# Performance work log

Hardware: AMD Instinct MI355X
Metric: run time of the kernel (lower is better)

## Reference

```python
import jax, jax.numpy as jnp
import numpy as np

BETA = 0.25
NUM_EMBEDS = 1024
EMBED_DIM = 256


def setup_inputs() -> dict:
    key = jax.random.key(0)
    k1, k2 = jax.random.split(key)
    z_e = jax.random.normal(k1, (32, EMBED_DIM, 1024), dtype=jnp.float32)
    lim = 1.0 / NUM_EMBEDS
    embed_weight = jax.random.uniform(k2, (NUM_EMBEDS, EMBED_DIM), dtype=jnp.float32,
                                      minval=-lim, maxval=lim)
    return {"z_e": z_e, "embed_weight": embed_weight}


def reference(z_e, embed_weight):
    # z_e: (b, d, t) -> (b, t, d)
    ze = jnp.transpose(z_e, (0, 2, 1))
    b, t, d = ze.shape
    flat = ze.reshape(-1, d)  # (N, d)
    K = embed_weight.shape[0]
    # squared euclidean distances (N, K) via sum-of-squares + matmul
    distances = (jnp.sum(flat ** 2, axis=1, keepdims=True)
                 + jnp.sum(embed_weight ** 2, axis=1)
                 - 2.0 * flat @ embed_weight.T)
    idx = jnp.argmin(distances, axis=1)  # (N,)
    # one-hot @ W is just a gather
    z_q = embed_weight[idx].reshape(b, t, d)
    # commitment / codebook losses (mse over all elements)
    e_latent_loss = jnp.mean((jax.lax.stop_gradient(z_q) - ze) ** 2)
    q_latent_loss = jnp.mean((z_q - jax.lax.stop_gradient(ze)) ** 2)
    reg_loss = q_latent_loss + BETA * e_latent_loss
    # straight-through estimator
    z_q_st = ze + jax.lax.stop_gradient(z_q - ze)
    z_q_out = jnp.transpose(z_q_st, (0, 2, 1))  # (b, d, t)
    # perplexity from codebook usage
    N = flat.shape[0]
    avg_probs = jnp.zeros((K,), dtype=jnp.float32).at[idx].add(1.0) / N
    perplexity = jnp.exp(-jnp.sum(avg_probs * jnp.log(avg_probs + 1e-10)))
    return (z_q_out, reg_loss, perplexity)
```

## Files before the change

### kernel.cpp

```cpp
#include <hip/hip_runtime.h>
#include <math.h>

#define BB 32
#define DD 256
#define TT 1024
#define KK 1024
#define NN (BB*TT)

#define BROWS 128
#define NSTEP 32


__global__ void prep_kernel(const float* __restrict__ W, float* __restrict__ wsq,
                            int* __restrict__ counts, float* __restrict__ sse) {
    const int k = blockIdx.x;
    const int lane = threadIdx.x;
    const float4 v = ((const float4*)(W + (size_t)k * DD))[lane];
    double s = (double)v.x * v.x + (double)v.y * v.y + (double)v.z * v.z + (double)v.w * v.w;
    #pragma unroll
    for (int m = 32; m > 0; m >>= 1) s += __shfl_down(s, m);
    if (lane == 0) wsq[k] = (float)s;
    if (blockIdx.x < 16) counts[blockIdx.x * 64 + lane] = 0;
    if (blockIdx.x == 0 && lane == 0) *sse = 0.0f;
}

__device__ __forceinline__ void gl_lds16(const float* g, void* l) {
    __builtin_amdgcn_global_load_lds((const __attribute__((address_space(1))) void*)g,
                                     (__attribute__((address_space(3))) void*)l, 16, 0, 0);
}

__global__ __launch_bounds__(512, 2) void vq_fused_kernel(
    const float* __restrict__ z, const float* __restrict__ W,
    const float* __restrict__ wsq, float* __restrict__ out,
    int* __restrict__ counts, float* __restrict__ sse)
{
    __shared__ float zst[2][16 * 128];
    __shared__ float wst[2][16 * 512];
    __shared__ float rsql[128];
    const int tid = threadIdx.x;
    const int wid = tid >> 6, lane = tid & 63;
    const int row0 = blockIdx.x * BROWS;
    const int b = row0 >> 10, t0 = row0 & 1023;
    const size_t bbase = (size_t)b * DD * TT;
    const float* zbase = z + bbase + t0;

    {
        char* dw = (char*)&wst[0][0];
        #pragma unroll
        for (int k = 0; k < 4; ++k) {
            const int m = k * 512 + tid;
            const int j = m >> 8, q = (m >> 6) & 3, l = m & 63;
            gl_lds16(W + (size_t)(j * 64 + l) * DD + q * 4, dw + (size_t)m * 16);
        }
        const int d = tid >> 5, r4 = (tid & 31) * 4;
        gl_lds16(zbase + (size_t)d * TT + r4, (char*)&zst[0][0] + (size_t)tid * 16);
    }

    {
        double* pscr = (double*)&zst[1][0];
        const int rr = tid & 127, g = tid >> 7;
        const float* zp = zbase + (size_t)g * 64 * TT + rr;
        double s = 0.0;
        #pragma unroll 4
        for (int d = 0; d < 64; ++d) { float v = zp[(size_t)d * TT]; s += (double)v * v; }
        pscr[g * 128 + rr] = s;
        __syncthreads();
        if (tid < 128)
            rsql[tid] = (float)((pscr[tid] + pscr[128 + tid]) + (pscr[256 + tid] + pscr[384 + tid]));
    }

    float minv[16]; int mini[16];
    #pragma unroll
    for (int i = 0; i < 16; ++i) { minv[i] = 3.4e38f; mini[i] = 0; }
    float acc[16][8];

    for (int t = 0; t < NSTEP; ++t) {
        const int ch = t >> 4, sl = t & 15, h = t & 1;
        __syncthreads();
        if (t + 1 < NSTEP) {
            const int tn = t + 1, chn = tn >> 4, sln = tn & 15;
            const float* wc = W + (size_t)(chn * 512) * DD + sln * 16;
            char* dw = (char*)&wst[tn & 1][0];
            #pragma unroll
            for (int k = 0; k < 4; ++k) {
                const int m = k * 512 + tid;
                const int j = m >> 8, q = (m >> 6) & 3, l = m & 63;
                gl_lds16(wc + (size_t)(j * 64 + l) * DD + q * 4, dw + (size_t)m * 16);
            }
            const int d = tid >> 5, r4 = (tid & 31) * 4;
            gl_lds16(zbase + (size_t)(sln * 16 + d) * TT + r4,
                     (char*)&zst[tn & 1][0] + (size_t)tid * 16);
        }
        if (sl == 0) {
            #pragma unroll
            for (int i = 0; i < 16; ++i)
                #pragma unroll
                for (int j = 0; j < 8; ++j) acc[i][j] = 0.0f;
        }
        const float*  zb  = &zst[h][0];
        const float4* wb4 = (const float4*)&wst[h][0];
        __builtin_amdgcn_s_setprio(1);
        #pragma clang loop unroll(disable)
        for (int q = 0; q < 4; ++q) {
            const float4* wp = wb4 + q * 64 + lane;
            float4 wf[8];
            #pragma unroll
            for (int j = 0; j < 8; ++j) wf[j] = wp[j * 256];
            #pragma unroll
            for (int dp = 0; dp < 4; ++dp) {
                const float4* zp4 = (const float4*)(zb + (q * 4 + dp) * 128 + wid * 16);
                const float4 za = zp4[0], zc = zp4[1], ze = zp4[2], zg = zp4[3];
                #pragma unroll
                for (int j = 0; j < 8; ++j) {
                    const float wv = dp == 0 ? wf[j].x : dp == 1 ? wf[j].y
                                   : dp == 2 ? wf[j].z : wf[j].w;
                    acc[0][j]  = fmaf(za.x, wv, acc[0][j]);
                    acc[1][j]  = fmaf(za.y, wv, acc[1][j]);
                    acc[2][j]  = fmaf(za.z, wv, acc[2][j]);
                    acc[3][j]  = fmaf(za.w, wv, acc[3][j]);
                    acc[4][j]  = fmaf(zc.x, wv, acc[4][j]);
                    acc[5][j]  = fmaf(zc.y, wv, acc[5][j]);
                    acc[6][j]  = fmaf(zc.z, wv, acc[6][j]);
                    acc[7][j]  = fmaf(zc.w, wv, acc[7][j]);
                    acc[8][j]  = fmaf(ze.x, wv, acc[8][j]);
                    acc[9][j]  = fmaf(ze.y, wv, acc[9][j]);
                    acc[10][j] = fmaf(ze.z, wv, acc[10][j]);
                    acc[11][j] = fmaf(ze.w, wv, acc[11][j]);
                    acc[12][j] = fmaf(zg.x, wv, acc[12][j]);
                    acc[13][j] = fmaf(zg.y, wv, acc[13][j]);
                    acc[14][j] = fmaf(zg.z, wv, acc[14][j]);
                    acc[15][j] = fmaf(zg.w, wv, acc[15][j]);
                }
            }
        }
        __builtin_amdgcn_s_setprio(0);
        if (sl == 15) {
            float wq[8];
            #pragma unroll
            for (int j = 0; j < 8; ++j) wq[j] = wsq[ch * 512 + j * 64 + lane];
            #pragma unroll
            for (int i = 0; i < 16; ++i) {
                const float rs = rsql[wid * 16 + i];
                #pragma unroll
                for (int j = 0; j < 8; ++j) {
                    const float s1 = rs + wq[j];
                    const float v = fmaf(-2.0f, acc[i][j], s1);
                    if (v < minv[i]) { minv[i] = v; mini[i] = ch * 512 + j * 64 + lane; }
                }
            }
        }
    }

    __syncthreads();
    int* idxs = (int*)&zst[0][0];
    float* ssescr = (float*)&wst[0][0];
    #pragma unroll
    for (int i = 0; i < 16; ++i) {
        float v = minv[i]; int ix = mini[i];
        #pragma unroll
        for (int m = 1; m < 64; m <<= 1) {
            float ov = __shfl_xor(v, m);
            int   oi = __shfl_xor(ix, m);
            if (ov < v || (ov == v && oi < ix)) { v = ov; ix = oi; }
        }
        if (lane == 0) {
            idxs[wid * 16 + i] = ix;
            atomicAdd(&counts[ix], 1);
        }
    }
    __syncthreads();

    const int tg = tid & 31;
    const int dg = tid >> 5;
    const int t4 = tg * 4;
    int ixs[4];
    #pragma unroll
    for (int m = 0; m < 4; ++m) ixs[m] = idxs[t4 + m];
    float ssel = 0.0f;
    #pragma unroll
    for (int k4 = 0; k4 < 4; ++k4) {
        const int d0 = dg * 16 + k4 * 4;
        float wr[4][4];
        #pragma unroll
        for (int m = 0; m < 4; ++m) {
            float4 wv = *(const float4*)(W + (size_t)ixs[m] * DD + d0);
            wr[m][0] = wv.x; wr[m][1] = wv.y; wr[m][2] = wv.z; wr[m][3] = wv.w;
        }
        #pragma unroll
        for (int dd = 0; dd < 4; ++dd) {
            const int d = d0 + dd;
            const size_t base = bbase + (size_t)d * TT + t0 + t4;
            float4 zv = *(const float4*)(z + base);
            float e0 = wr[0][dd] - zv.x, e1 = wr[1][dd] - zv.y;
            float e2 = wr[2][dd] - zv.z, e3 = wr[3][dd] - zv.w;
            float4 o;
            o.x = zv.x + e0; o.y = zv.y + e1; o.z = zv.z + e2; o.w = zv.w + e3;
            *(float4*)(out + base) = o;
            ssel += (e0 * e0 + e1 * e1) + (e2 * e2 + e3 * e3);
        }
    }
    #pragma unroll
    for (int m = 32; m > 0; m >>= 1) ssel += __shfl_down(ssel, m);
    if (lane == 0) ssescr[wid] = ssel;
    __syncthreads();
    if (tid == 0)
        atomicAdd(sse, ((ssescr[0] + ssescr[1]) + (ssescr[2] + ssescr[3]))
                     + ((ssescr[4] + ssescr[5]) + (ssescr[6] + ssescr[7])));
}

__global__ void finalize_kernel(const int* __restrict__ counts, const float* __restrict__ sse,
                                float* __restrict__ out) {
    float s = 0.0f;
    for (int k = threadIdx.x; k < KK; k += 256) {
        float p = (float)counts[k] / (float)NN;
        s += p * logf(p + 1e-10f);
    }
    #pragma unroll
    for (int m = 32; m > 0; m >>= 1) s += __shfl_down(s, m);
    __shared__ float wsum[4];
    if ((threadIdx.x & 63) == 0) wsum[threadIdx.x >> 6] = s;
    __syncthreads();
    if (threadIdx.x == 0) {
        float ent = (wsum[0] + wsum[1]) + (wsum[2] + wsum[3]);
        out[(size_t)BB * DD * TT]     = 1.25f * (*sse) / (float)(BB * DD * TT);
        out[(size_t)BB * DD * TT + 1] = expf(-ent);
    }
}

extern "C" void kernel_launch(void* const* d_in, const int* in_sizes, int n_in,
                              void* d_out, int out_size, void* d_ws, size_t ws_size,
                              hipStream_t stream) {
    const float* z = (const float*)d_in[0];
    const float* W = (const float*)d_in[1];
    float* out = (float*)d_out;

    float* wsq    = (float*)d_ws;
    int*   counts = (int*)(wsq + 1024);
    float* sse    = (float*)(counts + 1024);

    prep_kernel<<<1024, 64, 0, stream>>>(W, wsq, counts, sse);
    vq_fused_kernel<<<NN / BROWS, 512, 0, stream>>>(z, W, wsq, out, counts, sse);
    finalize_kernel<<<1, 256, 0, stream>>>(counts, sse, out);
}
```

Before: 228.5 us.

## Overlap row-norm computation with distance GEMM loop and unroll inner q loop

Removes the up-front strided loads that computed each row's squared norm before the main loop. The loads are now spread across the first 13 pipeline steps: issued before the FMA block and accumulated in double after it. Partial sums go to a dedicated LDS scratch and are reduced at step 13, before the first argmin at step 15. The inner q loop is also unrolled by two, which raises register pressure under the 512-thread, 2-block launch bounds and could cause spills.

```diff
diff --git a/kernel.cpp b/kernel.cpp
--- a/kernel.cpp
+++ b/kernel.cpp
@@ -36,6 +36,7 @@
 {
     __shared__ float zst[2][16 * 128];
     __shared__ float wst[2][16 * 512];
+    __shared__ double pscr[512];
     __shared__ float rsql[128];
     const int tid = threadIdx.x;
     const int wid = tid >> 6, lane = tid & 63;
@@ -56,18 +57,8 @@
         gl_lds16(zbase + (size_t)d * TT + r4, (char*)&zst[0][0] + (size_t)tid * 16);
     }
 
-    {
-        double* pscr = (double*)&zst[1][0];
-        const int rr = tid & 127, g = tid >> 7;
-        const float* zp = zbase + (size_t)g * 64 * TT + rr;
-        double s = 0.0;
-        #pragma unroll 4
-        for (int d = 0; d < 64; ++d) { float v = zp[(size_t)d * TT]; s += (double)v * v; }
-        pscr[g * 128 + rr] = s;
-        __syncthreads();
-        if (tid < 128)
-            rsql[tid] = (float)((pscr[tid] + pscr[128 + tid]) + (pscr[256 + tid] + pscr[384 + tid]));
-    }
+    const float* zrow = zbase + (size_t)(tid >> 7) * 64 * TT + (tid & 127);
+    double rchain = 0.0;
 
     float minv[16]; int mini[16];
     #pragma unroll
@@ -91,6 +82,19 @@
             gl_lds16(zbase + (size_t)(sln * 16 + d) * TT + r4,
                      (char*)&zst[tn & 1][0] + (size_t)tid * 16);
         }
+        float rv[5];
+        if (t < 13) {
+            #pragma unroll
+            for (int k = 0; k < 5; ++k) {
+                const int d = t * 5 + k;
+                if (d < 64) rv[k] = zrow[(size_t)d * TT];
+            }
+        }
+        if (sl == 13) {
+            if (tid < 128)
+                rsql[tid] = (float)((pscr[tid] + pscr[128 + tid])
+                                  + (pscr[256 + tid] + pscr[384 + tid]));
+        }
         if (sl == 0) {
             #pragma unroll
             for (int i = 0; i < 16; ++i)
@@ -100,7 +104,7 @@
         const float*  zb  = &zst[h][0];
         const float4* wb4 = (const float4*)&wst[h][0];
         __builtin_amdgcn_s_setprio(1);
-        #pragma clang loop unroll(disable)
+        #pragma clang loop unroll_count(2)
         for (int q = 0; q < 4; ++q) {
             const float4* wp = wb4 + q * 64 + lane;
             float4 wf[8];
@@ -134,6 +138,14 @@
             }
         }
         __builtin_amdgcn_s_setprio(0);
+        if (t < 13) {
+            #pragma unroll
+            for (int k = 0; k < 5; ++k) {
+                const int d = t * 5 + k;
+                if (d < 64) rchain += (double)rv[k] * rv[k];
+            }
+            if (t == 12) pscr[tid] = rchain;
+        }
         if (sl == 15) {
             float wq[8];
             #pragma unroll
```

Result: slower. 272.5 us (+19.3%).

## Triple-buffer LDS staging with explicit vmcnt waits and single barrier per step

Applied to the files above, without the earlier changes.

Moves the shared-memory staging of codebook and input slices from double to triple buffering, prefetching two steps ahead. Explicit s_waitcnt vmcnt counts plus a raw s_barrier at the end of each step replace the leading __syncthreads, so loads issued for later steps can stay in flight across the barrier. The codebook squared norms are loaded into registers once before the loop rather than at each chunk end. The extra buffer raises LDS use, which may limit residency of two blocks per CU, and the hand-counted vmcnt values must match the number of async loads issued.

```diff
diff --git a/kernel.cpp b/kernel.cpp
--- a/kernel.cpp
+++ b/kernel.cpp
@@ -34,8 +34,8 @@
     const float* __restrict__ wsq, float* __restrict__ out,
     int* __restrict__ counts, float* __restrict__ sse)
 {
-    __shared__ float zst[2][16 * 128];
-    __shared__ float wst[2][16 * 512];
+    __shared__ float zst[3][16 * 128];
+    __shared__ float wst[3][16 * 512];
     __shared__ float rsql[128];
     const int tid = threadIdx.x;
     const int wid = tid >> 6, lane = tid & 63;
@@ -44,20 +44,23 @@
     const size_t bbase = (size_t)b * DD * TT;
     const float* zbase = z + bbase + t0;
 
-    {
-        char* dw = (char*)&wst[0][0];
+    #pragma unroll
+    for (int pt = 0; pt < 2; ++pt) {
+        const float* wc = W + (size_t)0 * DD + pt * 16;
+        char* dw = (char*)&wst[pt][0];
         #pragma unroll
         for (int k = 0; k < 4; ++k) {
             const int m = k * 512 + tid;
             const int j = m >> 8, q = (m >> 6) & 3, l = m & 63;
-            gl_lds16(W + (size_t)(j * 64 + l) * DD + q * 4, dw + (size_t)m * 16);
+            gl_lds16(wc + (size_t)(j * 64 + l) * DD + q * 4, dw + (size_t)m * 16);
         }
         const int d = tid >> 5, r4 = (tid & 31) * 4;
-        gl_lds16(zbase + (size_t)d * TT + r4, (char*)&zst[0][0] + (size_t)tid * 16);
+        gl_lds16(zbase + (size_t)(pt * 16 + d) * TT + r4,
+                 (char*)&zst[pt][0] + (size_t)tid * 16);
     }
 
     {
-        double* pscr = (double*)&zst[1][0];
+        double* pscr = (double*)&wst[2][0];
         const int rr = tid & 127, g = tid >> 7;
         const float* zp = zbase + (size_t)g * 64 * TT + rr;
         double s = 0.0;
@@ -69,18 +72,27 @@
             rsql[tid] = (float)((pscr[tid] + pscr[128 + tid]) + (pscr[256 + tid] + pscr[384 + tid]));
     }
 
+    float wq0[8], wq1[8];
+    #pragma unroll
+    for (int j = 0; j < 8; ++j) {
+        wq0[j] = wsq[j * 64 + lane];
+        wq1[j] = wsq[512 + j * 64 + lane];
+    }
+
+    asm volatile("s_waitcnt vmcnt(0)" ::: "memory");
+    __syncthreads();
+
     float minv[16]; int mini[16];
     #pragma unroll
     for (int i = 0; i < 16; ++i) { minv[i] = 3.4e38f; mini[i] = 0; }
     float acc[16][8];
 
     for (int t = 0; t < NSTEP; ++t) {
-        const int ch = t >> 4, sl = t & 15, h = t & 1;
-        __syncthreads();
-        if (t + 1 < NSTEP) {
-            const int tn = t + 1, chn = tn >> 4, sln = tn & 15;
+        const int sl = t & 15, h = t % 3;
+        if (t + 2 < NSTEP) {
+            const int tn = t + 2, chn = tn >> 4, sln = tn & 15, hn = tn % 3;
             const float* wc = W + (size_t)(chn * 512) * DD + sln * 16;
-            char* dw = (char*)&wst[tn & 1][0];
+            char* dw = (char*)&wst[hn][0];
             #pragma unroll
             for (int k = 0; k < 4; ++k) {
                 const int m = k * 512 + tid;
@@ -89,7 +101,7 @@
             }
             const int d = tid >> 5, r4 = (tid & 31) * 4;
             gl_lds16(zbase + (size_t)(sln * 16 + d) * TT + r4,
-                     (char*)&zst[tn & 1][0] + (size_t)tid * 16);
+                     (char*)&zst[hn][0] + (size_t)tid * 16);
         }
         if (sl == 0) {
             #pragma unroll
@@ -134,21 +146,32 @@
             }
         }
         __builtin_amdgcn_s_setprio(0);
-        if (sl == 15) {
-            float wq[8];
-            #pragma unroll
-            for (int j = 0; j < 8; ++j) wq[j] = wsq[ch * 512 + j * 64 + lane];
+        if (t == 15) {
             #pragma unroll
             for (int i = 0; i < 16; ++i) {
                 const float rs = rsql[wid * 16 + i];
                 #pragma unroll
                 for (int j = 0; j < 8; ++j) {
-                    const float s1 = rs + wq[j];
+                    const float s1 = rs + wq0[j];
                     const float v = fmaf(-2.0f, acc[i][j], s1);
-                    if (v < minv[i]) { minv[i] = v; mini[i] = ch * 512 + j * 64 + lane; }
+                    if (v < minv[i]) { minv[i] = v; mini[i] = j * 64 + lane; }
                 }
             }
-        }
+        } else if (t == 31) {
+            #pragma unroll
+            for (int i = 0; i < 16; ++i) {
+                const float rs = rsql[wid * 16 + i];
+                #pragma unroll
+                for (int j = 0; j < 8; ++j) {
+                    const float s1 = rs + wq1[j];
+                    const float v = fmaf(-2.0f, acc[i][j], s1);
+                    if (v < minv[i]) { minv[i] = v; mini[i] = 512 + j * 64 + lane; }
+                }
+            }
+        }
+        if (t + 2 < NSTEP) { asm volatile("s_waitcnt vmcnt(5)" ::: "memory"); }
+        else               { asm volatile("s_waitcnt vmcnt(0)" ::: "memory"); }
+        __builtin_amdgcn_s_barrier();
     }
 
     __syncthreads();
```

Result: slower. 289.9 us (+26.9%).

## Double block to 1024 threads, halve per-thread rows, reduce argmin per chunk

Applied to the files above, without the earlier changes.

Launches the fused VQ kernel with 1024 threads per block. Each wave now owns 8 rows instead of 16, so the accumulator shrinks from 16x8 to 8x8 registers and occupancy can rise. The argmin across lanes now runs once per 512-code chunk, and the two chunk results are merged through shared memory, which removes the per-row running min registers. In exchange, each thread does less FMA work per LDS read of the W fragment, so the arithmetic intensity per LDS load drops, and the launch bounds of (1024,4) impose tight register limits that may cause spills.

```diff
diff --git a/kernel.cpp b/kernel.cpp
--- a/kernel.cpp
+++ b/kernel.cpp
@@ -29,7 +29,7 @@
                                      (__attribute__((address_space(3))) void*)l, 16, 0, 0);
 }
 
-__global__ __launch_bounds__(512, 2) void vq_fused_kernel(
+__global__ __launch_bounds__(1024, 4) void vq_fused_kernel(
     const float* __restrict__ z, const float* __restrict__ W,
     const float* __restrict__ wsq, float* __restrict__ out,
     int* __restrict__ counts, float* __restrict__ sse)
@@ -37,6 +37,9 @@
     __shared__ float zst[2][16 * 128];
     __shared__ float wst[2][16 * 512];
     __shared__ float rsql[128];
+    __shared__ float c0v[128];
+    __shared__ int   c0i[128];
+    __shared__ int   idxs[128];
     const int tid = threadIdx.x;
     const int wid = tid >> 6, lane = tid & 63;
     const int row0 = blockIdx.x * BROWS;
@@ -47,32 +50,33 @@
     {
         char* dw = (char*)&wst[0][0];
         #pragma unroll
-        for (int k = 0; k < 4; ++k) {
-            const int m = k * 512 + tid;
+        for (int k = 0; k < 2; ++k) {
+            const int m = k * 1024 + tid;
             const int j = m >> 8, q = (m >> 6) & 3, l = m & 63;
             gl_lds16(W + (size_t)(j * 64 + l) * DD + q * 4, dw + (size_t)m * 16);
         }
-        const int d = tid >> 5, r4 = (tid & 31) * 4;
-        gl_lds16(zbase + (size_t)d * TT + r4, (char*)&zst[0][0] + (size_t)tid * 16);
+        if (tid < 512) {
+            const int d = tid >> 5, r4 = (tid & 31) * 4;
+            gl_lds16(zbase + (size_t)d * TT + r4, (char*)&zst[0][0] + (size_t)tid * 16);
+        }
     }
 
     {
         double* pscr = (double*)&zst[1][0];
-        const int rr = tid & 127, g = tid >> 7;
-        const float* zp = zbase + (size_t)g * 64 * TT + rr;
-        double s = 0.0;
-        #pragma unroll 4
-        for (int d = 0; d < 64; ++d) { float v = zp[(size_t)d * TT]; s += (double)v * v; }
-        pscr[g * 128 + rr] = s;
+        if (tid < 512) {
+            const int rr = tid & 127, g = (tid >> 7) & 3;
+            const float* zp = zbase + (size_t)g * 64 * TT + rr;
+            double s = 0.0;
+            #pragma unroll 4
+            for (int d = 0; d < 64; ++d) { float v = zp[(size_t)d * TT]; s += (double)v * v; }
+            pscr[g * 128 + rr] = s;
+        }
         __syncthreads();
         if (tid < 128)
             rsql[tid] = (float)((pscr[tid] + pscr[128 + tid]) + (pscr[256 + tid] + pscr[384 + tid]));
     }
 
-    float minv[16]; int mini[16];
-    #pragma unroll
-    for (int i = 0; i < 16; ++i) { minv[i] = 3.4e38f; mini[i] = 0; }
-    float acc[16][8];
+    float acc[8][8];
 
     for (int t = 0; t < NSTEP; ++t) {
         const int ch = t >> 4, sl = t & 15, h = t & 1;
@@ -82,18 +86,20 @@
             const float* wc = W + (size_t)(chn * 512) * DD + sln * 16;
             char* dw = (char*)&wst[tn & 1][0];
             #pragma unroll
-            for (int k = 0; k < 4; ++k) {
-                const int m = k * 512 + tid;
+            for (int k = 0; k < 2; ++k) {
+                const int m = k * 1024 + tid;
                 const int j = m >> 8, q = (m >> 6) & 3, l = m & 63;
                 gl_lds16(wc + (size_t)(j * 64 + l) * DD + q * 4, dw + (size_t)m * 16);
             }
-            const int d = tid >> 5, r4 = (tid & 31) * 4;
-            gl_lds16(zbase + (size_t)(sln * 16 + d) * TT + r4,
-                     (char*)&zst[tn & 1][0] + (size_t)tid * 16);
+            if (tid < 512) {
+                const int d = tid >> 5, r4 = (tid & 31) * 4;
+                gl_lds16(zbase + (size_t)(sln * 16 + d) * TT + r4,
+                         (char*)&zst[tn & 1][0] + (size_t)tid * 16);
+            }
         }
         if (sl == 0) {
             #pragma unroll
-            for (int i = 0; i < 16; ++i)
+            for (int i = 0; i < 8; ++i)
                 #pragma unroll
                 for (int j = 0; j < 8; ++j) acc[i][j] = 0.0f;
         }
@@ -108,28 +114,20 @@
             for (int j = 0; j < 8; ++j) wf[j] = wp[j * 256];
             #pragma unroll
             for (int dp = 0; dp < 4; ++dp) {
-                const float4* zp4 = (const float4*)(zb + (q * 4 + dp) * 128 + wid * 16);
-                const float4 za = zp4[0], zc = zp4[1], ze = zp4[2], zg = zp4[3];
+                const float4* zp4 = (const float4*)(zb + (q * 4 + dp) * 128 + wid * 8);
+                const float4 za = zp4[0], zc = zp4[1];
                 #pragma unroll
                 for (int j = 0; j < 8; ++j) {
                     const float wv = dp == 0 ? wf[j].x : dp == 1 ? wf[j].y
                                    : dp == 2 ? wf[j].z : wf[j].w;
-                    acc[0][j]  = fmaf(za.x, wv, acc[0][j]);
-                    acc[1][j]  = fmaf(za.y, wv, acc[1][j]);
-                    acc[2][j]  = fmaf(za.z, wv, acc[2][j]);
-                    acc[3][j]  = fmaf(za.w, wv, acc[3][j]);
-                    acc[4][j]  = fmaf(zc.x, wv, acc[4][j]);
-                    acc[5][j]  = fmaf(zc.y, wv, acc[5][j]);
-                    acc[6][j]  = fmaf(zc.z, wv, acc[6][j]);
-                    acc[7][j]  = fmaf(zc.w, wv, acc[7][j]);
-                    acc[8][j]  = fmaf(ze.x, wv, acc[8][j]);
-                    acc[9][j]  = fmaf(ze.y, wv, acc[9][j]);
-                    acc[10][j] = fmaf(ze.z, wv, acc[10][j]);
-                    acc[11][j] = fmaf(ze.w, wv, acc[11][j]);
-                    acc[12][j] = fmaf(zg.x, wv, acc[12][j]);
-                    acc[13][j] = fmaf(zg.y, wv, acc[13][j]);
-                    acc[14][j] = fmaf(zg.z, wv, acc[14][j]);
-                    acc[15][j] = fmaf(zg.w, wv, acc[15][j]);
+                    acc[0][j] = fmaf(za.x, wv, acc[0][j]);
+                    acc[1][j] = fmaf(za.y, wv, acc[1][j]);
+                    acc[2][j] = fmaf(za.z, wv, acc[2][j]);
+                    acc[3][j] = fmaf(za.w, wv, acc[3][j]);
+                    acc[4][j] = fmaf(zc.x, wv, acc[4][j]);
+                    acc[5][j] = fmaf(zc.y, wv, acc[5][j]);
+                    acc[6][j] = fmaf(zc.z, wv, acc[6][j]);
+                    acc[7][j] = fmaf(zc.w, wv, acc[7][j]);
                 }
             }
         }
@@ -139,36 +137,36 @@
             #pragma unroll
             for (int j = 0; j < 8; ++j) wq[j] = wsq[ch * 512 + j * 64 + lane];
             #pragma unroll
-            for (int i = 0; i < 16; ++i) {
-                const float rs = rsql[wid * 16 + i];
+            for (int i = 0; i < 8; ++i) {
+                const float rs = rsql[wid * 8 + i];
+                float mv = 3.4e38f; int mi = 0;
                 #pragma unroll
                 for (int j = 0; j < 8; ++j) {
                     const float s1 = rs + wq[j];
                     const float v = fmaf(-2.0f, acc[i][j], s1);
-                    if (v < minv[i]) { minv[i] = v; mini[i] = ch * 512 + j * 64 + lane; }
+                    if (v < mv) { mv = v; mi = ch * 512 + j * 64 + lane; }
+                }
+                #pragma unroll
+                for (int m = 1; m < 64; m <<= 1) {
+                    float ov = __shfl_xor(mv, m);
+                    int   oi = __shfl_xor(mi, m);
+                    if (ov < mv || (ov == mv && oi < mi)) { mv = ov; mi = oi; }
+                }
+                if (lane == 0) {
+                    const int row = wid * 8 + i;
+                    if (ch == 0) { c0v[row] = mv; c0i[row] = mi; }
+                    else {
+                        int fi = (mv < c0v[row]) ? mi : c0i[row];
+                        idxs[row] = fi;
+                        atomicAdd(&counts[fi], 1);
+                    }
                 }
             }
         }
     }
 
     __syncthreads();
-    int* idxs = (int*)&zst[0][0];
     float* ssescr = (float*)&wst[0][0];
-    #pragma unroll
-    for (int i = 0; i < 16; ++i) {
-        float v = minv[i]; int ix = mini[i];
-        #pragma unroll
-        for (int m = 1; m < 64; m <<= 1) {
-            float ov = __shfl_xor(v, m);
-            int   oi = __shfl_xor(ix, m);
-            if (ov < v || (ov == v && oi < ix)) { v = ov; ix = oi; }
-        }
-        if (lane == 0) {
-            idxs[wid * 16 + i] = ix;
-            atomicAdd(&counts[ix], 1);
-        }
-    }
-    __syncthreads();
 
     const int tg = tid & 31;
     const int dg = tid >> 5;
@@ -178,8 +176,8 @@
     for (int m = 0; m < 4; ++m) ixs[m] = idxs[t4 + m];
     float ssel = 0.0f;
     #pragma unroll
-    for (int k4 = 0; k4 < 4; ++k4) {
-        const int d0 = dg * 16 + k4 * 4;
+    for (int k4 = 0; k4 < 2; ++k4) {
+        const int d0 = dg * 8 + k4 * 4;
         float wr[4][4];
         #pragma unroll
         for (int m = 0; m < 4; ++m) {
@@ -203,9 +201,13 @@
     for (int m = 32; m > 0; m >>= 1) ssel += __shfl_down(ssel, m);
     if (lane == 0) ssescr[wid] = ssel;
     __syncthreads();
-    if (tid == 0)
-        atomicAdd(sse, ((ssescr[0] + ssescr[1]) + (ssescr[2] + ssescr[3]))
-                     + ((ssescr[4] + ssescr[5]) + (ssescr[6] + ssescr[7])));
+    if (tid == 0) {
+        float s0 = ((ssescr[0] + ssescr[1]) + (ssescr[2] + ssescr[3]))
+                 + ((ssescr[4] + ssescr[5]) + (ssescr[6] + ssescr[7]));
+        float s1 = ((ssescr[8] + ssescr[9]) + (ssescr[10] + ssescr[11]))
+                 + ((ssescr[12] + ssescr[13]) + (ssescr[14] + ssescr[15]));
+        atomicAdd(sse, s0 + s1);
+    }
 }
 
 __global__ void finalize_kernel(const int* __restrict__ counts, const float* __restrict__ sse,
@@ -239,6 +241,6 @@
     float* sse    = (float*)(counts + 1024);
 
     prep_kernel<<<1024, 64, 0, stream>>>(W, wsq, counts, sse);
-    vq_fused_kernel<<<NN / BROWS, 512, 0, stream>>>(z, W, wsq, out, counts, sse);
+    vq_fused_kernel<<<NN / BROWS, 1024, 0, stream>>>(z, W, wsq, out, counts, sse);
     finalize_kernel<<<1, 256, 0, stream>>>(counts, sse, out);
 }
```

After: 317.5 us. 39.0% more time.
